# Kernel optimization log

Measured on AMD Instinct MI355X. Metric: run time of the kernel, lower is better.

The kernel has to match this reference:

```python
import jax, jax.numpy as jnp
import numpy as np

N, E, G = 100000, 1600000, 8
IN, H, OUT = 3, 64, 20


def setup_inputs() -> dict:
    key = jax.random.key(0)
    ks = jax.random.split(key, 24)
    def nrm(k, shape, scale=0.1):
        return jax.random.normal(k, shape, dtype=jnp.float32) * scale
    inp = {}
    inp["x"] = jax.random.normal(ks[0], (N, IN), dtype=jnp.float32)
    inp["edge_index"] = jax.random.randint(ks[1], (2, E), 0, N, dtype=jnp.int32)
    inp["batch"] = jnp.sort(jax.random.randint(ks[2], (N,), 0, G, dtype=jnp.int32))
    dims = [(IN, H), (H, H), (H, H)]  # 3 GATConv layers (initial + layers-1)
    for i, (di, do) in enumerate(dims):
        inp[f"W{i}"] = nrm(ks[3 + 4 * i], (di, do))
        inp[f"as{i}"] = nrm(ks[4 + 4 * i], (do,))
        inp[f"ad{i}"] = nrm(ks[5 + 4 * i], (do,))
        inp[f"b{i}"] = jnp.zeros((do,), jnp.float32)
    inp["vn_emb0"] = jnp.zeros((1, H), jnp.float32)  # constant-0 init per module
    inp["m1_w1"] = nrm(ks[15], (H, H)); inp["m1_b1"] = jnp.zeros((H,), jnp.float32)
    inp["m1_w2"] = nrm(ks[16], (H, H)); inp["m1_b2"] = jnp.zeros((H,), jnp.float32)
    inp["mf_w1"] = nrm(ks[17], (H, H)); inp["mf_b1"] = jnp.zeros((H,), jnp.float32)
    inp["mf_w2"] = nrm(ks[18], (H, OUT)); inp["mf_b2"] = jnp.zeros((OUT,), jnp.float32)
    inp["out_w"] = nrm(ks[19], (H, OUT)); inp["out_b"] = jnp.zeros((OUT,), jnp.float32)
    return inp


def _gat(x, src, dst, W, a_s, a_d, b):
    # PyG GATConv, 1 head: h = xW; e_ij = LeakyReLU_0.2(a_s.h_j + a_d.h_i);
    # alpha = softmax over incoming edges of each dst node; out_i = sum_j alpha_ij h_j + b
    h = x @ W                                                  # [N, H]
    lg = jax.nn.leaky_relu((h @ a_s)[src] + (h @ a_d)[dst], 0.2)  # [E+N]
    m = jax.ops.segment_max(lg, dst, num_segments=N)
    m = jnp.where(jnp.isfinite(m), m, 0.0)
    p = jnp.exp(lg - m[dst])
    denom = jax.ops.segment_sum(p, dst, num_segments=N)
    alpha = p / denom[dst]
    return jax.ops.segment_sum(alpha[:, None] * h[src], dst, num_segments=N) + b


def _forward(x, edge_index, batch, params):
    (W0, as0, ad0, b0, W1, as1, ad1, b1, W2, as2, ad2, b2,
     vn_emb0, m1_w1, m1_b1, m1_w2, m1_b2, mf_w1, mf_b1, mf_w2, mf_b2,
     out_w, out_b) = params
    loops = jnp.arange(N, dtype=edge_index.dtype)  # GATConv add_self_loops=True
    src = jnp.concatenate([edge_index[0], loops])
    dst = jnp.concatenate([edge_index[1], loops])
    act = lambda v: jax.nn.leaky_relu(v, 0.01)  # nn.LeakyReLU default slope
    h = act(_gat(x, src, dst, W0, as0, ad0, b0))
    h = act(_gat(h, src, dst, W1, as1, ad1, b1))
    h = act(_gat(h, src, dst, W2, as2, ad2, b2))
    # virtual node: global_add_pool(out, batch) + Embedding(0) (zero-init)
    vn = jax.ops.segment_sum(h, batch, num_segments=G) + vn_emb0[0]
    vn = jax.nn.relu(vn @ m1_w1 + m1_b1)
    vn = jax.nn.relu(vn @ m1_w2 + m1_b2)
    vn = jax.nn.relu(vn @ mf_w1 + mf_b1)
    vn = jax.nn.relu(vn @ mf_w2 + mf_b2)
    return (h @ out_w + out_b, vn)


def reference(x, edge_index, batch, W0, as0, ad0, b0, W1, as1, ad1, b1,
              W2, as2, ad2, b2, vn_emb0, m1_w1, m1_b1, m1_w2, m1_b2,
              mf_w1, mf_b1, mf_w2, mf_b2, out_w, out_b):
    params = (W0, as0, ad0, b0, W1, as1, ad1, b1, W2, as2, ad2, b2,
              vn_emb0, m1_w1, m1_b1, m1_w2, m1_b2, mf_w1, mf_b1, mf_w2, mf_b2,
              out_w, out_b)
    return _forward(x, edge_index, batch, params)
```

## Files before the change

### kernel.cpp

```cpp
#include <hip/hip_runtime.h>
#include <hip/hip_bf16.h>

#define H 64
#define OUTD 20
#define NGRAPH 8
#define NBK 256
#define CAPB 8192
#define MAXDEG 63

typedef __attribute__((ext_vector_type(8))) short bf16x8;
typedef __attribute__((ext_vector_type(4))) float f32x4;
typedef __attribute__((ext_vector_type(8))) unsigned short u16x8;


__device__ __forceinline__ float ldp(const void* p, int i, bool f32) {
    return f32 ? ((const float*)p)[i]
               : __bfloat162float(((const __hip_bfloat16*)p)[i]);
}

__device__ __forceinline__ float bfu(unsigned short u) {
    union { unsigned int i; float f; } c; c.i = ((unsigned)u) << 16; return c.f;
}
__device__ __forceinline__ unsigned short fbits(float f) {
    __hip_bfloat16 b = __float2bfloat16(f);
    return *reinterpret_cast<unsigned short*>(&b);
}

__global__ void detect_dtype(const unsigned short* __restrict__ xb, int n_u16,
                             int* __restrict__ flag) {
    __shared__ int sh[256];
    int t = threadIdx.x;
    int m = min(n_u16, 4096);
    int bad = 0;
    for (int i = t; i < m; i += 256) {
        unsigned e = (xb[i] >> 7) & 0xFF;
        bad += (e >= 0x90) ? 1 : 0;
    }
    sh[t] = bad;
    __syncthreads();
    for (int off = 128; off; off >>= 1) {
        if (t < off) sh[t] += sh[t + off];
        __syncthreads();
    }
    if (t == 0) *flag = (sh[0] > (m >> 4)) ? 1 : 0;
}

__global__ void fillC_dense0(const int* __restrict__ src, const int* __restrict__ dst,
                             int* __restrict__ gcur, unsigned* __restrict__ ebuf,
                             int E, int n, int nC, int EPC, int nbk,
                             const void* __restrict__ x, const void* __restrict__ W,
                             const void* __restrict__ a_s, const void* __restrict__ a_d,
                             __hip_bfloat16* __restrict__ h, float* __restrict__ s,
                             float* __restrict__ d, const int* __restrict__ flagp) {
    if ((int)blockIdx.x < nC) {
        __shared__ unsigned lcnt[NBK];
        __shared__ int lbase[NBK];
        int t = threadIdx.x;
        for (int i = t; i < NBK; i += 256) lcnt[i] = 0;
        __syncthreads();
        int base = blockIdx.x * (256 * EPC) + t;
        for (int i = 0; i < EPC; ++i) {
            int e = base + i * 256;
            if (e < E) {
                int dn = dst[e];
                if ((unsigned)dn < (unsigned)n) atomicAdd(&lcnt[dn >> 9], 1u);
            }
        }
        __syncthreads();
        for (int i = t; i < nbk; i += 256) {
            unsigned c = lcnt[i];
            lbase[i] = c ? atomicAdd(&gcur[i], (int)c) : 0;
            lcnt[i] = 0;
        }
        __syncthreads();
        for (int i = 0; i < EPC; ++i) {
            int e = base + i * 256;
            if (e < E) {
                int dn = dst[e];
                if ((unsigned)dn < (unsigned)n) {
                    int b = dn >> 9;
                    unsigned pos = (unsigned)lbase[b] + atomicAdd(&lcnt[b], 1u);
                    if (pos < CAPB)
                        ebuf[(size_t)b * CAPB + pos] =
                            ((unsigned)src[e] << 9) | (unsigned)(dn & 511);
                }
            }
        }
        return;
    }
    const bool f32 = (*flagp != 0);
    int idx = ((int)blockIdx.x - nC) * 256 + threadIdx.x;
    int node = idx >> 6;
    int f = idx & 63;
    if (node >= n) return;
    float acc = 0.f;
    for (int k = 0; k < 3; ++k)
        acc += ldp(x, node * 3 + k, f32) * ldp(W, k * H + f, f32);
    ((short*)h)[((size_t)(f >> 5) * n + node) * 32 + (f & 31)] = (short)fbits(acc);
    float sv = acc * ldp(a_s, f, f32);
    float dv = acc * ldp(a_d, f, f32);
    for (int off = 32; off; off >>= 1) {
        sv += __shfl_xor(sv, off);
        dv += __shfl_xor(dv, off);
    }
    if (f == 0) { s[node] = sv; d[node] = dv; }
}

__global__ __launch_bounds__(512) void bucketD(const unsigned* __restrict__ ebuf,
                                               const int* __restrict__ gcur,
                                               unsigned* __restrict__ cntoff,
                                               int* __restrict__ col,
                                               int* __restrict__ gtot, int n) {
    __shared__ unsigned lcnt[512];
    __shared__ int loff[512];
    __shared__ int sc[512];
    __shared__ int sdeg[512];
    __shared__ int sbase;
    int b = blockIdx.x, t = threadIdx.x;
    lcnt[t] = 0;
    __syncthreads();
    int end = min(gcur[b], CAPB);
    const unsigned* reg = ebuf + (size_t)b * CAPB;
    for (int i = t; i < end; i += 512) atomicAdd(&lcnt[reg[i] & 511u], 1u);
    __syncthreads();
    int node = (b << 9) + t;
    int degc = (node < n) ? (int)min(lcnt[t], (unsigned)MAXDEG) : -1;
    int slots = degc + 1;
    sc[t] = slots;
    __syncthreads();
    for (int ofs = 1; ofs < 512; ofs <<= 1) {
        int v = (t >= ofs) ? sc[t - ofs] : 0;
        __syncthreads();
        sc[t] += v;
        __syncthreads();
    }
    if (t == 511) sbase = atomicAdd(gtot, sc[511]);
    __syncthreads();
    int myoff = sbase + sc[t] - slots;
    int dg = (degc > 0) ? degc : 0;
    loff[t] = myoff;
    sdeg[t] = dg;
    if (node < n) cntoff[node] = (unsigned)myoff | ((unsigned)dg << 24);
    lcnt[t] = 0;
    __syncthreads();
    for (int i = t; i < end; i += 512) {
        unsigned e = reg[i];
        int loc = (int)(e & 511u);
        unsigned pos = atomicAdd(&lcnt[loc], 1u);
        if ((int)pos < sdeg[loc])
            col[loff[loc] + pos] = (int)(e >> 9);
    }
}

#define ACC8(w, hv) { \
    a[0] += w * bfu(hv[0]); a[1] += w * bfu(hv[1]); \
    a[2] += w * bfu(hv[2]); a[3] += w * bfu(hv[3]); \
    a[4] += w * bfu(hv[4]); a[5] += w * bfu(hv[5]); \
    a[6] += w * bfu(hv[6]); a[7] += w * bfu(hv[7]); }

__global__ void gat_agg_sliced(const short* __restrict__ hs,
                               const float* __restrict__ s,
                               const float* __restrict__ d,
                               const unsigned* __restrict__ cntoff,
                               const int* __restrict__ col,
                               const void* __restrict__ bias,
                               short* __restrict__ outs, int n,
                               const int* __restrict__ flagp) {
    const bool f32 = (*flagp != 0);
    int shp = (int)blockIdx.x & 7;
    int fh = shp >> 2, nq = shp & 3;
    int qN = (n + 3) >> 2;
    int node = nq * qN + ((int)blockIdx.x >> 3) * 8 + ((int)threadIdx.x >> 5);
    int lim = min(n, (nq + 1) * qN);
    if (node >= lim) return;
    int l = threadIdx.x & 31;
    int c = l & 3, q = l >> 2;
    unsigned co = cntoff[node];
    int deg = (int)(co >> 24);
    int D = deg + 1;
    const int* cb = col + (co & 0xFFFFFFu);
    const u16x8* h8 = (const u16x8*)hs + (size_t)fh * n * 4 + c;
    float di = d[node];

    int e0 = q, e1 = q + 8, e2 = q + 16;
    int s0 = cb[min(e0, deg)];
    int s1 = cb[min(e1, deg)];
    int s2 = cb[min(e2, deg)];
    s0 = (e0 < deg) ? s0 : node;
    s1 = (e1 < deg) ? s1 : node;
    s2 = (e2 < deg) ? s2 : node;
    if ((unsigned)s0 >= (unsigned)n) s0 = 0;
    if ((unsigned)s1 >= (unsigned)n) s1 = 0;
    if ((unsigned)s2 >= (unsigned)n) s2 = 0;
    float v0 = s[s0] + di, v1 = s[s1] + di, v2 = s[s2] + di;
    u16x8 hv0 = h8[(size_t)s0 * 4];
    u16x8 hv1 = h8[(size_t)s1 * 4];
    u16x8 hv2 = h8[(size_t)s2 * 4];
    v0 = v0 > 0.f ? v0 : 0.2f * v0;
    v1 = v1 > 0.f ? v1 : 0.2f * v1;
    v2 = v2 > 0.f ? v2 : 0.2f * v2;
    float sv0 = (e0 < D) ? v0 : -INFINITY;
    float sv1 = (e1 < D) ? v1 : -INFINITY;
    float sv2 = (e2 < D) ? v2 : -INFINITY;

    float sv3 = -INFINITY, sv4 = -INFINITY, sv5 = -INFINITY,
          sv6 = -INFINITY, sv7 = -INFINITY;
    u16x8 hv3 = {}, hv4 = {}, hv5 = {}, hv6 = {}, hv7 = {};
    bool big = (D > 24);
    if (big) {
        int e3 = q + 24, e4 = q + 32, e5 = q + 40, e6 = q + 48, e7 = q + 56;
        int s3 = cb[min(e3, deg)];
        int s4 = cb[min(e4, deg)];
        int s5 = cb[min(e5, deg)];
        int s6 = cb[min(e6, deg)];
        int s7 = cb[min(e7, deg)];
        s3 = (e3 < deg) ? s3 : node;
        s4 = (e4 < deg) ? s4 : node;
        s5 = (e5 < deg) ? s5 : node;
        s6 = (e6 < deg) ? s6 : node;
        s7 = (e7 < deg) ? s7 : node;
        if ((unsigned)s3 >= (unsigned)n) s3 = 0;
        if ((unsigned)s4 >= (unsigned)n) s4 = 0;
        if ((unsigned)s5 >= (unsigned)n) s5 = 0;
        if ((unsigned)s6 >= (unsigned)n) s6 = 0;
        if ((unsigned)s7 >= (unsigned)n) s7 = 0;
        float w3 = s[s3] + di, w4 = s[s4] + di, w5 = s[s5] + di,
              w6 = s[s6] + di, w7 = s[s7] + di;
        hv3 = h8[(size_t)s3 * 4];
        hv4 = h8[(size_t)s4 * 4];
        hv5 = h8[(size_t)s5 * 4];
        hv6 = h8[(size_t)s6 * 4];
        hv7 = h8[(size_t)s7 * 4];
        w3 = w3 > 0.f ? w3 : 0.2f * w3;
        w4 = w4 > 0.f ? w4 : 0.2f * w4;
        w5 = w5 > 0.f ? w5 : 0.2f * w5;
        w6 = w6 > 0.f ? w6 : 0.2f * w6;
        w7 = w7 > 0.f ? w7 : 0.2f * w7;
        sv3 = (e3 < D) ? w3 : -INFINITY;
        sv4 = (e4 < D) ? w4 : -INFINITY;
        sv5 = (e5 < D) ? w5 : -INFINITY;
        sv6 = (e6 < D) ? w6 : -INFINITY;
        sv7 = (e7 < D) ? w7 : -INFINITY;
    }

    float mx = fmaxf(fmaxf(fmaxf(sv0, sv1), fmaxf(sv2, sv3)),
                     fmaxf(fmaxf(sv4, sv5), fmaxf(sv6, sv7)));
    mx = fmaxf(mx, __shfl_xor(mx, 4));
    mx = fmaxf(mx, __shfl_xor(mx, 8));
    mx = fmaxf(mx, __shfl_xor(mx, 16));

    float w0 = __expf(sv0 - mx);
    float w1 = __expf(sv1 - mx);
    float w2 = __expf(sv2 - mx);
    float wsum = w0 + w1 + w2;

    float a[8] = {0.f, 0.f, 0.f, 0.f, 0.f, 0.f, 0.f, 0.f};
    ACC8(w0, hv0);
    ACC8(w1, hv1);
    ACC8(w2, hv2);
    if (big) {
        float w3 = __expf(sv3 - mx);
        float w4 = __expf(sv4 - mx);
        float w5 = __expf(sv5 - mx);
        float w6 = __expf(sv6 - mx);
        float w7 = __expf(sv7 - mx);
        wsum += w3 + w4 + w5 + w6 + w7;
        ACC8(w3, hv3);
        ACC8(w4, hv4);
        ACC8(w5, hv5);
        ACC8(w6, hv6);
        ACC8(w7, hv7);
    }
    wsum += __shfl_xor(wsum, 4);
    wsum += __shfl_xor(wsum, 8);
    wsum += __shfl_xor(wsum, 16);
#pragma unroll
    for (int i = 0; i < 8; ++i) {
        a[i] += __shfl_xor(a[i], 4);
        a[i] += __shfl_xor(a[i], 8);
        a[i] += __shfl_xor(a[i], 16);
    }
    if (q == 0) {
        float inv = 1.f / fmaxf(wsum, 1e-20f);
        u16x8 ov;
        for (int i = 0; i < 8; ++i) {
            float o = a[i] * inv + ldp(bias, fh * 32 + c * 8 + i, f32);
            o = o > 0.f ? o : 0.01f * o;
            ov[i] = fbits(o);
        }
        ((u16x8*)outs)[((size_t)fh * n + node) * 4 + c] = ov;
    }
}


__global__ __launch_bounds__(256) void denseN_mfma(
    const __hip_bfloat16* __restrict__ in,
    const void* __restrict__ W,
    const void* __restrict__ a_s, const void* __restrict__ a_d,
    __hip_bfloat16* __restrict__ h, float* __restrict__ s,
    float* __restrict__ d, int n, const int* __restrict__ flagp) {
    const bool f32 = (*flagp != 0);
    __shared__ short Wt[64 * 72];
    int t = threadIdx.x;
    for (int i = t; i < 4096; i += 256) {
        int k = i >> 6, nf = i & 63;
        Wt[nf * 72 + k] = (short)fbits(ldp(W, i, f32));
    }
    __syncthreads();

    int wid = t >> 6, lane = t & 63;
    int quad = lane >> 4, n16 = lane & 15;
    int nodeBase = blockIdx.x * 64 + wid * 16;
    int mrow = nodeBase + n16;
    int mclamp = min(mrow, n - 1);
    const short* inp = (const short*)in;
    bf16x8 a0 = *(const bf16x8*)(inp + (size_t)mclamp * 32 + quad * 8);
    bf16x8 a1 = *(const bf16x8*)(inp + ((size_t)n + mclamp) * 32 + quad * 8);

    float as_v[4], ad_v[4];
    for (int nt = 0; nt < 4; ++nt) {
        as_v[nt] = ldp(a_s, nt * 16 + n16, f32);
        ad_v[nt] = ldp(a_d, nt * 16 + n16, f32);
    }

    float sv[4] = {0.f, 0.f, 0.f, 0.f}, dv[4] = {0.f, 0.f, 0.f, 0.f};
    f32x4 accs[4];
    for (int nt = 0; nt < 4; ++nt) {
        const short* wrow = Wt + (nt * 16 + n16) * 72;
        bf16x8 b0 = *(const bf16x8*)(wrow + quad * 8);
        bf16x8 b1 = *(const bf16x8*)(wrow + 32 + quad * 8);
        f32x4 cacc = {0.f, 0.f, 0.f, 0.f};
        cacc = __builtin_amdgcn_mfma_f32_16x16x32_bf16(a0, b0, cacc, 0, 0, 0);
        cacc = __builtin_amdgcn_mfma_f32_16x16x32_bf16(a1, b1, cacc, 0, 0, 0);
        accs[nt] = cacc;
        for (int r = 0; r < 4; ++r) {
            sv[r] += cacc[r] * as_v[nt];
            dv[r] += cacc[r] * ad_v[nt];
        }
    }

    short* hb = (short*)h;
    for (int r = 0; r < 4; ++r) {
        int node = nodeBase + quad * 4 + r;
        if (node < n) {
            for (int nt = 0; nt < 4; ++nt) {
                int f = nt * 16 + n16;
                hb[((size_t)(f >> 5) * n + node) * 32 + (f & 31)] = (short)fbits(accs[nt][r]);
            }
        }
    }
    for (int r = 0; r < 4; ++r) {
        for (int mask = 1; mask < 16; mask <<= 1) {
            sv[r] += __shfl_xor(sv[r], mask);
            dv[r] += __shfl_xor(dv[r], mask);
        }
    }
    if (n16 == 0) {
        for (int r = 0; r < 4; ++r) {
            int node = nodeBase + quad * 4 + r;
            if (node < n) { s[node] = sv[r]; d[node] = dv[r]; }
        }
    }
}


__global__ __launch_bounds__(256) void proj_pool(
    const __hip_bfloat16* __restrict__ h,
    const void* __restrict__ W, const void* __restrict__ b,
    void* __restrict__ out, int n, const int* __restrict__ flagp,
    int projBlocks, const int* __restrict__ batch, float* __restrict__ vn) {
    const bool f32 = (*flagp != 0);
    if ((int)blockIdx.x < projBlocks) {
        __shared__ short Wt[32 * 72];
        int t = threadIdx.x;
        for (int i = t; i < 32 * 64; i += 256) {
            int o = i >> 6, k = i & 63;
            Wt[o * 72 + k] = (o < OUTD) ? (short)fbits(ldp(W, k * OUTD + o, f32)) : 0;
        }
        __syncthreads();

        int wid = t >> 6, lane = t & 63;
        int quad = lane >> 4, n16 = lane & 15;
        int nodeBase = blockIdx.x * 64 + wid * 16;
        int mclamp = min(nodeBase + n16, n - 1);
        const short* hsrc = (const short*)h;
        bf16x8 a0 = *(const bf16x8*)(hsrc + (size_t)mclamp * 32 + quad * 8);
        bf16x8 a1 = *(const bf16x8*)(hsrc + ((size_t)n + mclamp) * 32 + quad * 8);

        f32x4 acc0 = {0.f, 0.f, 0.f, 0.f}, acc1 = {0.f, 0.f, 0.f, 0.f};
        {
            const short* wrow = Wt + n16 * 72;
            bf16x8 b0 = *(const bf16x8*)(wrow + quad * 8);
            bf16x8 b1 = *(const bf16x8*)(wrow + 32 + quad * 8);
            acc0 = __builtin_amdgcn_mfma_f32_16x16x32_bf16(a0, b0, acc0, 0, 0, 0);
            acc0 = __builtin_amdgcn_mfma_f32_16x16x32_bf16(a1, b1, acc0, 0, 0, 0);
        }
        {
            const short* wrow = Wt + (16 + n16) * 72;
            bf16x8 b0 = *(const bf16x8*)(wrow + quad * 8);
            bf16x8 b1 = *(const bf16x8*)(wrow + 32 + quad * 8);
            acc1 = __builtin_amdgcn_mfma_f32_16x16x32_bf16(a0, b0, acc1, 0, 0, 0);
            acc1 = __builtin_amdgcn_mfma_f32_16x16x32_bf16(a1, b1, acc1, 0, 0, 0);
        }
        float bv0 = ldp(b, n16, f32);
        float bv1 = (n16 < OUTD - 16) ? ldp(b, 16 + n16, f32) : 0.f;
        for (int r = 0; r < 4; ++r) {
            int node = nodeBase + quad * 4 + r;
            if (node >= n) break;
            float o0 = acc0[r] + bv0;
            if (f32) ((float*)out)[node * OUTD + n16] = o0;
            else     ((__hip_bfloat16*)out)[node * OUTD + n16] = __float2bfloat16(o0);
            if (n16 < OUTD - 16) {
                float o1 = acc1[r] + bv1;
                if (f32) ((float*)out)[node * OUTD + 16 + n16] = o1;
                else     ((__hip_bfloat16*)out)[node * OUTD + 16 + n16] = __float2bfloat16(o1);
            }
        }
        return;
    }
    __shared__ float part[NGRAPH * H];
    int t = threadIdx.x;
    for (int i = t; i < NGRAPH * H; i += 256) part[i] = 0.f;
    __syncthreads();
    int pb = (int)blockIdx.x - projBlocks;
    int npb = gridDim.x - projBlocks;
    int wid = t >> 6, lane = t & 63;
    int gwave = pb * 4 + wid;
    int nwaves = npb * 4;
    int chunk = (n + nwaves - 1) / nwaves;
    int beg = gwave * chunk;
    int end = min(n, beg + chunk);
    if (beg < end) {
        const short* hb = (const short*)h + (size_t)(lane >> 5) * n * 32 + (lane & 31);
        float acc = 0.f;
        int cur = batch[beg];
        for (int i = beg; i < end; ++i) {
            int g = batch[i];
            if (g != cur) {
                if ((unsigned)cur < NGRAPH) atomicAdd(&part[cur * H + lane], acc);
                acc = 0.f;
                cur = g;
            }
            acc += bfu((unsigned short)hb[(size_t)i * 32]);
        }
        if ((unsigned)cur < NGRAPH) atomicAdd(&part[cur * H + lane], acc);
    }
    __syncthreads();
    for (int i = t; i < NGRAPH * H; i += 256) {
        float v = part[i];
        if (v != 0.f) atomicAdd(&vn[i], v);
    }
}


__global__ void vn_mlp(const float* __restrict__ vn, const void* __restrict__ emb,
                       const void* __restrict__ w1, const void* __restrict__ b1,
                       const void* __restrict__ w2, const void* __restrict__ b2,
                       const void* __restrict__ w3, const void* __restrict__ b3,
                       const void* __restrict__ w4, const void* __restrict__ b4,
                       void* __restrict__ out, int out1_off, const int* __restrict__ flagp) {
    const bool f32 = (*flagp != 0);
    __shared__ float A[NGRAPH * H], B[NGRAPH * H];
    int t = threadIdx.x;
    int g = t >> 6, f = t & 63;
    A[t] = vn[t] + ldp(emb, f, f32);
    __syncthreads();
    float acc = ldp(b1, f, f32);
    for (int k = 0; k < H; ++k) acc += A[g * H + k] * ldp(w1, k * H + f, f32);
    B[t] = fmaxf(acc, 0.f);
    __syncthreads();
    acc = ldp(b2, f, f32);
    for (int k = 0; k < H; ++k) acc += B[g * H + k] * ldp(w2, k * H + f, f32);
    A[t] = fmaxf(acc, 0.f);
    __syncthreads();
    acc = ldp(b3, f, f32);
    for (int k = 0; k < H; ++k) acc += A[g * H + k] * ldp(w3, k * H + f, f32);
    B[t] = fmaxf(acc, 0.f);
    __syncthreads();
    if (f < OUTD) {
        acc = ldp(b4, f, f32);
        for (int k = 0; k < H; ++k) acc += B[g * H + k] * ldp(w4, k * OUTD + f, f32);
        acc = fmaxf(acc, 0.f);
        int idx = out1_off + g * OUTD + f;
        if (f32) ((float*)out)[idx] = acc;
        else     ((__hip_bfloat16*)out)[idx] = __float2bfloat16(acc);
    }
}


extern "C" void kernel_launch(void* const* d_in, const int* in_sizes, int n_in,
                              void* d_out, int out_size, void* d_ws, size_t ws_size,
                              hipStream_t stream) {
    const void* x   = d_in[0];
    const int* ei   = (const int*)d_in[1];
    const int* batch= (const int*)d_in[2];
    const void* W0  = d_in[3];
    const void* as0 = d_in[4];
    const void* ad0 = d_in[5];
    const void* b0  = d_in[6];
    const void* W1  = d_in[7];
    const void* as1 = d_in[8];
    const void* ad1 = d_in[9];
    const void* b1  = d_in[10];
    const void* W2  = d_in[11];
    const void* as2 = d_in[12];
    const void* ad2 = d_in[13];
    const void* b2  = d_in[14];
    const void* vne = d_in[15];
    const void* m1w1 = d_in[16];
    const void* m1b1 = d_in[17];
    const void* m1w2 = d_in[18];
    const void* m1b2 = d_in[19];
    const void* mfw1 = d_in[20];
    const void* mfb1 = d_in[21];
    const void* mfw2 = d_in[22];
    const void* mfb2 = d_in[23];
    const void* outw = d_in[24];
    const void* outb = d_in[25];

    const int N = in_sizes[2];
    const int E = in_sizes[1] / 2;
    const int* srcp = ei;
    const int* dstp = ei + E;

    char* w = (char*)d_ws;
    auto alloc = [&](size_t bytes) -> void* {
        void* p = (void*)w;
        w += ((bytes + 255) / 256) * 256;
        return p;
    };
    int*   flag   = (int*)alloc(256);
    int*   gcur   = (int*)alloc((size_t)NBK * 4);
    int*   gtot   = (int*)alloc(256);
    unsigned* ebuf= (unsigned*)alloc((size_t)NBK * CAPB * 4);
    unsigned* cntoff = (unsigned*)alloc((size_t)N * 4);
    int*   col    = (int*)alloc(((size_t)E + N + 64) * 4);
    __hip_bfloat16* featA = (__hip_bfloat16*)alloc((size_t)N * H * 2);
    __hip_bfloat16* featB = (__hip_bfloat16*)alloc((size_t)N * H * 2);
    __hip_bfloat16* hbuf  = (__hip_bfloat16*)alloc((size_t)N * H * 2);
    float* sArr   = (float*)alloc((size_t)N * 4);
    float* dArr   = (float*)alloc((size_t)N * 4);
    float* vn     = (float*)alloc((size_t)NGRAPH * H * 4);

    const int nbN64 = (N * H + 255) / 256;
    const int nb64 = (N + 63) / 64;
    const int projBlocks = (N + 63) / 64;
    const int nbk = (N + 511) >> 9;
    const int qN = (N + 3) >> 2;
    const int aggBlocks = 8 * ((qN + 7) / 8);
    int EPC = 8;
    int nC = (E + 256 * EPC - 1) / (256 * EPC);
    while (nC > 1024) { EPC <<= 1; nC = (E + 256 * EPC - 1) / (256 * EPC); }

    detect_dtype<<<1, 256, 0, stream>>>((const unsigned short*)x, in_sizes[0], flag);

    hipMemsetAsync(gcur, 0, (size_t)NBK * 4, stream);
    hipMemsetAsync(gtot, 0, 4, stream);
    hipMemsetAsync(vn, 0, (size_t)NGRAPH * H * 4, stream);
    fillC_dense0<<<nC + nbN64, 256, 0, stream>>>(
        srcp, dstp, gcur, ebuf, E, N, nC, EPC, nbk,
        x, W0, as0, ad0, hbuf, sArr, dArr, flag);
    bucketD<<<nbk, 512, 0, stream>>>(ebuf, gcur, cntoff, col, gtot, N);

    gat_agg_sliced<<<aggBlocks, 256, 0, stream>>>((const short*)hbuf, sArr, dArr,
                                                  cntoff, col, b0, (short*)featA, N, flag);
    denseN_mfma<<<nb64, 256, 0, stream>>>(featA, W1, as1, ad1, hbuf, sArr, dArr, N, flag);
    gat_agg_sliced<<<aggBlocks, 256, 0, stream>>>((const short*)hbuf, sArr, dArr,
                                                  cntoff, col, b1, (short*)featB, N, flag);
    denseN_mfma<<<nb64, 256, 0, stream>>>(featB, W2, as2, ad2, hbuf, sArr, dArr, N, flag);
    gat_agg_sliced<<<aggBlocks, 256, 0, stream>>>((const short*)hbuf, sArr, dArr,
                                                  cntoff, col, b2, (short*)featA, N, flag);

    proj_pool<<<projBlocks + 512, 256, 0, stream>>>(featA, outw, outb, d_out, N, flag,
                                                    projBlocks, batch, vn);
    vn_mlp<<<1, 512, 0, stream>>>(vn, vne, m1w1, m1b1, m1w2, m1b2, mfw1, mfb1, mfw2, mfb2,
                                  d_out, N * OUTD, flag);
}
```

Before: 425.5 us.

## Pad CSR rows with sentinel node to remove per-edge bounds checks in aggregation

Each node's neighbour list is now padded to a multiple of 8 (or 64 for large degrees) and the padding points to an extra sentinel row N, whose feature row is zero and whose score is -1e30. The self loop is written explicitly into the list, so the aggregation kernel loads indices directly with no min/clamp/select logic, and skips later groups based on the padded count. The feature buffers gain a stride of N+1 to hold the sentinel row. The separate memsets are folded into the dtype-detect kernel, which cuts launches. The cost is a larger col array, an extra fill pass over the padding in bucketD, and some extra gathers of the sentinel row.

```diff
diff --git a/kernel.cpp b/kernel.cpp
--- a/kernel.cpp
+++ b/kernel.cpp
@@ -27,7 +27,10 @@
 }
 
 __global__ void detect_dtype(const unsigned short* __restrict__ xb, int n_u16,
-                             int* __restrict__ flag) {
+                             int* __restrict__ flag, int* __restrict__ gcur,
+                             int* __restrict__ gtot, float* __restrict__ vnp,
+                             float* __restrict__ s, short* __restrict__ hbuf,
+                             int n, int ns) {
     __shared__ int sh[256];
     int t = threadIdx.x;
     int m = min(n_u16, 4096);
@@ -37,6 +40,11 @@
         bad += (e >= 0x90) ? 1 : 0;
     }
     sh[t] = bad;
+    if (t < NBK) gcur[t] = 0;
+    for (int i = t; i < NGRAPH * H; i += 256) vnp[i] = 0.f;
+    if (t < 32) hbuf[(size_t)n * 32 + t] = 0;
+    else if (t < 64) hbuf[((size_t)ns + n) * 32 + (t - 32)] = 0;
+    if (t == 0) { *gtot = 0; s[n] = -1e30f; }
     __syncthreads();
     for (int off = 128; off; off >>= 1) {
         if (t < off) sh[t] += sh[t + off];
@@ -47,7 +55,7 @@
 
 __global__ void fillC_dense0(const int* __restrict__ src, const int* __restrict__ dst,
                              int* __restrict__ gcur, unsigned* __restrict__ ebuf,
-                             int E, int n, int nC, int EPC, int nbk,
+                             int E, int n, int ns, int nC, int EPC, int nbk,
                              const void* __restrict__ x, const void* __restrict__ W,
                              const void* __restrict__ a_s, const void* __restrict__ a_d,
                              __hip_bfloat16* __restrict__ h, float* __restrict__ s,
@@ -96,7 +104,7 @@
     float acc = 0.f;
     for (int k = 0; k < 3; ++k)
         acc += ldp(x, node * 3 + k, f32) * ldp(W, k * H + f, f32);
-    ((short*)h)[((size_t)(f >> 5) * n + node) * 32 + (f & 31)] = (short)fbits(acc);
+    ((short*)h)[((size_t)(f >> 5) * ns + node) * 32 + (f & 31)] = (short)fbits(acc);
     float sv = acc * ldp(a_s, f, f32);
     float dv = acc * ldp(a_d, f, f32);
     for (int off = 32; off; off >>= 1) {
@@ -124,9 +132,10 @@
     for (int i = t; i < end; i += 512) atomicAdd(&lcnt[reg[i] & 511u], 1u);
     __syncthreads();
     int node = (b << 9) + t;
-    int degc = (node < n) ? (int)min(lcnt[t], (unsigned)MAXDEG) : -1;
-    int slots = degc + 1;
-    sc[t] = slots;
+    int degc = (node < n) ? (int)min(lcnt[t], (unsigned)MAXDEG) : 0;
+    int d1 = degc + 1;
+    int Dp = (node < n) ? ((d1 <= 24) ? ((d1 + 7) & ~7) : 64) : 0;
+    sc[t] = Dp;
     __syncthreads();
     for (int ofs = 1; ofs < 512; ofs <<= 1) {
         int v = (t >= ofs) ? sc[t - ofs] : 0;
@@ -136,13 +145,16 @@
     }
     if (t == 511) sbase = atomicAdd(gtot, sc[511]);
     __syncthreads();
-    int myoff = sbase + sc[t] - slots;
-    int dg = (degc > 0) ? degc : 0;
+    int myoff = sbase + sc[t] - Dp;
     loff[t] = myoff;
-    sdeg[t] = dg;
-    if (node < n) cntoff[node] = (unsigned)myoff | ((unsigned)dg << 24);
+    sdeg[t] = degc;
+    if (node < n) cntoff[node] = (unsigned)myoff | ((unsigned)Dp << 24);
     lcnt[t] = 0;
     __syncthreads();
+    int total = sc[511];
+    for (int i = t; i < total; i += 512) col[sbase + i] = n;
+    __syncthreads();
+    if (node < n) col[myoff + degc] = node;
     for (int i = t; i < end; i += 512) {
         unsigned e = reg[i];
         int loc = (int)(e & 511u);
@@ -164,7 +176,7 @@
                                const unsigned* __restrict__ cntoff,
                                const int* __restrict__ col,
                                const void* __restrict__ bias,
-                               short* __restrict__ outs, int n,
+                               short* __restrict__ outs, int n, int ns,
                                const int* __restrict__ flagp) {
     const bool f32 = (*flagp != 0);
     int shp = (int)blockIdx.x & 7;
@@ -176,71 +188,54 @@
     int l = threadIdx.x & 31;
     int c = l & 3, q = l >> 2;
     unsigned co = cntoff[node];
-    int deg = (int)(co >> 24);
-    int D = deg + 1;
+    int Dp = (int)(co >> 24);
     const int* cb = col + (co & 0xFFFFFFu);
-    const u16x8* h8 = (const u16x8*)hs + (size_t)fh * n * 4 + c;
+    const char* hb = (const char*)hs + (size_t)fh * ns * 64;
     float di = d[node];
-
-    int e0 = q, e1 = q + 8, e2 = q + 16;
-    int s0 = cb[min(e0, deg)];
-    int s1 = cb[min(e1, deg)];
-    int s2 = cb[min(e2, deg)];
-    s0 = (e0 < deg) ? s0 : node;
-    s1 = (e1 < deg) ? s1 : node;
-    s2 = (e2 < deg) ? s2 : node;
-    if ((unsigned)s0 >= (unsigned)n) s0 = 0;
-    if ((unsigned)s1 >= (unsigned)n) s1 = 0;
-    if ((unsigned)s2 >= (unsigned)n) s2 = 0;
-    float v0 = s[s0] + di, v1 = s[s1] + di, v2 = s[s2] + di;
-    u16x8 hv0 = h8[(size_t)s0 * 4];
-    u16x8 hv1 = h8[(size_t)s1 * 4];
-    u16x8 hv2 = h8[(size_t)s2 * 4];
-    v0 = v0 > 0.f ? v0 : 0.2f * v0;
-    v1 = v1 > 0.f ? v1 : 0.2f * v1;
-    v2 = v2 > 0.f ? v2 : 0.2f * v2;
-    float sv0 = (e0 < D) ? v0 : -INFINITY;
-    float sv1 = (e1 < D) ? v1 : -INFINITY;
-    float sv2 = (e2 < D) ? v2 : -INFINITY;
+    unsigned coff = (unsigned)c * 16u;
+
+    int s0 = cb[q];
+    float v0 = s[s0] + di;
+    u16x8 hv0 = *(const u16x8*)(hb + ((unsigned)s0 * 64u + coff));
+    float sv0 = v0 > 0.f ? v0 : 0.2f * v0;
+
+    float sv1 = -INFINITY, sv2 = -INFINITY;
+    u16x8 hv1 = {}, hv2 = {};
+    if (Dp > 8) {
+        int s1 = cb[q + 8];
+        float v1 = s[s1] + di;
+        hv1 = *(const u16x8*)(hb + ((unsigned)s1 * 64u + coff));
+        sv1 = v1 > 0.f ? v1 : 0.2f * v1;
+    }
+    if (Dp > 16) {
+        int s2 = cb[q + 16];
+        float v2 = s[s2] + di;
+        hv2 = *(const u16x8*)(hb + ((unsigned)s2 * 64u + coff));
+        sv2 = v2 > 0.f ? v2 : 0.2f * v2;
+    }
 
     float sv3 = -INFINITY, sv4 = -INFINITY, sv5 = -INFINITY,
           sv6 = -INFINITY, sv7 = -INFINITY;
     u16x8 hv3 = {}, hv4 = {}, hv5 = {}, hv6 = {}, hv7 = {};
-    bool big = (D > 24);
+    bool big = (Dp > 24);
     if (big) {
-        int e3 = q + 24, e4 = q + 32, e5 = q + 40, e6 = q + 48, e7 = q + 56;
-        int s3 = cb[min(e3, deg)];
-        int s4 = cb[min(e4, deg)];
-        int s5 = cb[min(e5, deg)];
-        int s6 = cb[min(e6, deg)];
-        int s7 = cb[min(e7, deg)];
-        s3 = (e3 < deg) ? s3 : node;
-        s4 = (e4 < deg) ? s4 : node;
-        s5 = (e5 < deg) ? s5 : node;
-        s6 = (e6 < deg) ? s6 : node;
-        s7 = (e7 < deg) ? s7 : node;
-        if ((unsigned)s3 >= (unsigned)n) s3 = 0;
-        if ((unsigned)s4 >= (unsigned)n) s4 = 0;
-        if ((unsigned)s5 >= (unsigned)n) s5 = 0;
-        if ((unsigned)s6 >= (unsigned)n) s6 = 0;
-        if ((unsigned)s7 >= (unsigned)n) s7 = 0;
-        float w3 = s[s3] + di, w4 = s[s4] + di, w5 = s[s5] + di,
-              w6 = s[s6] + di, w7 = s[s7] + di;
-        hv3 = h8[(size_t)s3 * 4];
-        hv4 = h8[(size_t)s4 * 4];
-        hv5 = h8[(size_t)s5 * 4];
-        hv6 = h8[(size_t)s6 * 4];
-        hv7 = h8[(size_t)s7 * 4];
-        w3 = w3 > 0.f ? w3 : 0.2f * w3;
-        w4 = w4 > 0.f ? w4 : 0.2f * w4;
-        w5 = w5 > 0.f ? w5 : 0.2f * w5;
-        w6 = w6 > 0.f ? w6 : 0.2f * w6;
-        w7 = w7 > 0.f ? w7 : 0.2f * w7;
-        sv3 = (e3 < D) ? w3 : -INFINITY;
-        sv4 = (e4 < D) ? w4 : -INFINITY;
-        sv5 = (e5 < D) ? w5 : -INFINITY;
-        sv6 = (e6 < D) ? w6 : -INFINITY;
-        sv7 = (e7 < D) ? w7 : -INFINITY;
+        int s3 = cb[q + 24];
+        int s4 = cb[q + 32];
+        int s5 = cb[q + 40];
+        int s6 = cb[q + 48];
+        int s7 = cb[q + 56];
+        float v3 = s[s3] + di, v4 = s[s4] + di, v5 = s[s5] + di,
+              v6 = s[s6] + di, v7 = s[s7] + di;
+        hv3 = *(const u16x8*)(hb + ((unsigned)s3 * 64u + coff));
+        hv4 = *(const u16x8*)(hb + ((unsigned)s4 * 64u + coff));
+        hv5 = *(const u16x8*)(hb + ((unsigned)s5 * 64u + coff));
+        hv6 = *(const u16x8*)(hb + ((unsigned)s6 * 64u + coff));
+        hv7 = *(const u16x8*)(hb + ((unsigned)s7 * 64u + coff));
+        sv3 = v3 > 0.f ? v3 : 0.2f * v3;
+        sv4 = v4 > 0.f ? v4 : 0.2f * v4;
+        sv5 = v5 > 0.f ? v5 : 0.2f * v5;
+        sv6 = v6 > 0.f ? v6 : 0.2f * v6;
+        sv7 = v7 > 0.f ? v7 : 0.2f * v7;
     }
 
     float mx = fmaxf(fmaxf(fmaxf(sv0, sv1), fmaxf(sv2, sv3)),
@@ -288,7 +283,7 @@
             o = o > 0.f ? o : 0.01f * o;
             ov[i] = fbits(o);
         }
-        ((u16x8*)outs)[((size_t)fh * n + node) * 4 + c] = ov;
+        ((u16x8*)outs)[((size_t)fh * ns + node) * 4 + c] = ov;
     }
 }
 
@@ -298,7 +293,7 @@
     const void* __restrict__ W,
     const void* __restrict__ a_s, const void* __restrict__ a_d,
     __hip_bfloat16* __restrict__ h, float* __restrict__ s,
-    float* __restrict__ d, int n, const int* __restrict__ flagp) {
+    float* __restrict__ d, int n, int ns, const int* __restrict__ flagp) {
     const bool f32 = (*flagp != 0);
     __shared__ short Wt[64 * 72];
     int t = threadIdx.x;
@@ -315,7 +310,7 @@
     int mclamp = min(mrow, n - 1);
     const short* inp = (const short*)in;
     bf16x8 a0 = *(const bf16x8*)(inp + (size_t)mclamp * 32 + quad * 8);
-    bf16x8 a1 = *(const bf16x8*)(inp + ((size_t)n + mclamp) * 32 + quad * 8);
+    bf16x8 a1 = *(const bf16x8*)(inp + ((size_t)ns + mclamp) * 32 + quad * 8);
 
     float as_v[4], ad_v[4];
     for (int nt = 0; nt < 4; ++nt) {
@@ -345,7 +340,7 @@
         if (node < n) {
             for (int nt = 0; nt < 4; ++nt) {
                 int f = nt * 16 + n16;
-                hb[((size_t)(f >> 5) * n + node) * 32 + (f & 31)] = (short)fbits(accs[nt][r]);
+                hb[((size_t)(f >> 5) * ns + node) * 32 + (f & 31)] = (short)fbits(accs[nt][r]);
             }
         }
     }
@@ -367,7 +362,7 @@
 __global__ __launch_bounds__(256) void proj_pool(
     const __hip_bfloat16* __restrict__ h,
     const void* __restrict__ W, const void* __restrict__ b,
-    void* __restrict__ out, int n, const int* __restrict__ flagp,
+    void* __restrict__ out, int n, int ns, const int* __restrict__ flagp,
     int projBlocks, const int* __restrict__ batch, float* __restrict__ vn) {
     const bool f32 = (*flagp != 0);
     if ((int)blockIdx.x < projBlocks) {
@@ -385,7 +380,7 @@
         int mclamp = min(nodeBase + n16, n - 1);
         const short* hsrc = (const short*)h;
         bf16x8 a0 = *(const bf16x8*)(hsrc + (size_t)mclamp * 32 + quad * 8);
-        bf16x8 a1 = *(const bf16x8*)(hsrc + ((size_t)n + mclamp) * 32 + quad * 8);
+        bf16x8 a1 = *(const bf16x8*)(hsrc + ((size_t)ns + mclamp) * 32 + quad * 8);
 
         f32x4 acc0 = {0.f, 0.f, 0.f, 0.f}, acc1 = {0.f, 0.f, 0.f, 0.f};
         {
@@ -431,7 +426,7 @@
     int beg = gwave * chunk;
     int end = min(n, beg + chunk);
     if (beg < end) {
-        const short* hb = (const short*)h + (size_t)(lane >> 5) * n * 32 + (lane & 31);
+        const short* hb = (const short*)h + (size_t)(lane >> 5) * ns * 32 + (lane & 31);
         float acc = 0.f;
         int cur = batch[beg];
         for (int i = beg; i < end; ++i) {
@@ -520,6 +515,7 @@
 
     const int N = in_sizes[2];
     const int E = in_sizes[1] / 2;
+    const int NS = N + 1;
     const int* srcp = ei;
     const int* dstp = ei + E;
 
@@ -534,11 +530,11 @@
     int*   gtot   = (int*)alloc(256);
     unsigned* ebuf= (unsigned*)alloc((size_t)NBK * CAPB * 4);
     unsigned* cntoff = (unsigned*)alloc((size_t)N * 4);
-    int*   col    = (int*)alloc(((size_t)E + N + 64) * 4);
-    __hip_bfloat16* featA = (__hip_bfloat16*)alloc((size_t)N * H * 2);
-    __hip_bfloat16* featB = (__hip_bfloat16*)alloc((size_t)N * H * 2);
-    __hip_bfloat16* hbuf  = (__hip_bfloat16*)alloc((size_t)N * H * 2);
-    float* sArr   = (float*)alloc((size_t)N * 4);
+    int*   col    = (int*)alloc(((size_t)N * 64 + 64) * 4);
+    __hip_bfloat16* featA = (__hip_bfloat16*)alloc((size_t)NS * H * 2);
+    __hip_bfloat16* featB = (__hip_bfloat16*)alloc((size_t)NS * H * 2);
+    __hip_bfloat16* hbuf  = (__hip_bfloat16*)alloc((size_t)NS * H * 2);
+    float* sArr   = (float*)alloc((size_t)NS * 4);
     float* dArr   = (float*)alloc((size_t)N * 4);
     float* vn     = (float*)alloc((size_t)NGRAPH * H * 4);
 
@@ -552,26 +548,24 @@
     int nC = (E + 256 * EPC - 1) / (256 * EPC);
     while (nC > 1024) { EPC <<= 1; nC = (E + 256 * EPC - 1) / (256 * EPC); }
 
-    detect_dtype<<<1, 256, 0, stream>>>((const unsigned short*)x, in_sizes[0], flag);
-
-    hipMemsetAsync(gcur, 0, (size_t)NBK * 4, stream);
-    hipMemsetAsync(gtot, 0, 4, stream);
-    hipMemsetAsync(vn, 0, (size_t)NGRAPH * H * 4, stream);
+    detect_dtype<<<1, 256, 0, stream>>>((const unsigned short*)x, in_sizes[0], flag,
+                                        gcur, gtot, vn, sArr, (short*)hbuf, N, NS);
+
     fillC_dense0<<<nC + nbN64, 256, 0, stream>>>(
-        srcp, dstp, gcur, ebuf, E, N, nC, EPC, nbk,
+        srcp, dstp, gcur, ebuf, E, N, NS, nC, EPC, nbk,
         x, W0, as0, ad0, hbuf, sArr, dArr, flag);
     bucketD<<<nbk, 512, 0, stream>>>(ebuf, gcur, cntoff, col, gtot, N);
 
     gat_agg_sliced<<<aggBlocks, 256, 0, stream>>>((const short*)hbuf, sArr, dArr,
-                                                  cntoff, col, b0, (short*)featA, N, flag);
-    denseN_mfma<<<nb64, 256, 0, stream>>>(featA, W1, as1, ad1, hbuf, sArr, dArr, N, flag);
+                                                  cntoff, col, b0, (short*)featA, N, NS, flag);
+    denseN_mfma<<<nb64, 256, 0, stream>>>(featA, W1, as1, ad1, hbuf, sArr, dArr, N, NS, flag);
     gat_agg_sliced<<<aggBlocks, 256, 0, stream>>>((const short*)hbuf, sArr, dArr,
-                                                  cntoff, col, b1, (short*)featB, N, flag);
-    denseN_mfma<<<nb64, 256, 0, stream>>>(featB, W2, as2, ad2, hbuf, sArr, dArr, N, flag);
+                                                  cntoff, col, b1, (short*)featB, N, NS, flag);
+    denseN_mfma<<<nb64, 256, 0, stream>>>(featB, W2, as2, ad2, hbuf, sArr, dArr, N, NS, flag);
     gat_agg_sliced<<<aggBlocks, 256, 0, stream>>>((const short*)hbuf, sArr, dArr,
-                                                  cntoff, col, b2, (short*)featA, N, flag);
-
-    proj_pool<<<projBlocks + 512, 256, 0, stream>>>(featA, outw, outb, d_out, N, flag,
+                                                  cntoff, col, b2, (short*)featA, N, NS, flag);
+
+    proj_pool<<<projBlocks + 512, 256, 0, stream>>>(featA, outw, outb, d_out, N, NS, flag,
                                                     projBlocks, batch, vn);
     vn_mlp<<<1, 512, 0, stream>>>(vn, vne, m1w1, m1b1, m1w2, m1b2, mfw1, mfb1, mfw2, mfb2,
                                   d_out, N * OUTD, flag);
```

After: 442.4 us. 4.0% more time.
